# Kernel tuning notes

Measured on AMD Instinct MI355X. Metric: run time of the kernel, lower is better.

## Reference

```python
import jax, jax.numpy as jnp
import numpy as np

N_WORDS, L, VOCAB, D = 8192, 24, 128, 512
H, DK = 8, 64  # n_head, d_v (=d_k)
N_NAMES, WORDS_PER_NAME = 2048, 4
N_CONCEPTS, NAMES_PER_CONCEPT = 256, 8


def setup_inputs() -> dict:
    key = jax.random.key(0)
    ks = jax.random.split(key, 9)
    s = 1.0 / np.sqrt(D).astype(np.float32)
    inputs = jax.random.randint(ks[0], (N_WORDS, L), 0, VOCAB)  # 0 = pad char
    n_words = jnp.full((N_NAMES,), WORDS_PER_NAME, dtype=jnp.int32)
    n_names = jnp.full((N_CONCEPTS,), NAMES_PER_CONCEPT, dtype=jnp.int32)
    return {
        "inputs": inputs,
        "n_words": n_words,
        "n_names": n_names,
        "emb": jax.random.normal(ks[1], (VOCAB, D), jnp.float32) * s,
        "Wq": jax.random.normal(ks[2], (D, H * DK), jnp.float32) * s,
        "Wk": jax.random.normal(ks[3], (D, H * DK), jnp.float32) * s,
        "Wv": jax.random.normal(ks[4], (D, H * DK), jnp.float32) * s,
        "Wo": jax.random.normal(ks[5], (H * DK, D), jnp.float32) * s,
        "W1": jax.random.normal(ks[6], (D, 512), jnp.float32) * s,
        "W2": jax.random.normal(ks[7], (512, 256), jnp.float32) * s,
    }


def reference(inputs, n_words, n_names, emb, Wq, Wk, Wv, Wo, W1, W2):
    N, Lq = inputs.shape
    pad = inputs == 0  # [N, L] padding mask (char id 0)

    # --- MHAEncoder: embedding + masked multi-head self-attention ---
    x = emb[inputs]  # [N, L, D]
    def split_heads(t):  # [N, L, H*DK] -> [N, H, L, DK]
        return t.reshape(N, Lq, H, DK).transpose(0, 2, 1, 3)
    q = split_heads(x @ Wq)
    k = split_heads(x @ Wk)
    v = split_heads(x @ Wv)
    scale = jnp.asarray(1.0 / np.sqrt(DK), x.dtype)
    scores = jnp.einsum('nhqd,nhkd->nhqk', q, k) * scale  # [N, H, L, L]
    scores = jnp.where(pad[:, None, None, :], jnp.asarray(-1e9, x.dtype), scores)
    attn = jax.nn.softmax(scores, axis=-1)
    o = jnp.einsum('nhqk,nhkd->nhqd', attn, v)
    word_ft = o.transpose(0, 2, 1, 3).reshape(N, Lq, H * DK) @ Wo  # [N, L, D]

    # --- masked mean pooling over chars: matmul(mask, word_ft)/mask.sum(-1) ---
    m = (~pad).astype(word_ft.dtype)  # [N, L]
    name_emb = jnp.einsum('nl,nld->nd', m, word_ft) / m.sum(-1, keepdims=True)  # [N, D]

    # --- split(n_words) + per-group mean == segment mean over word groups ---
    G = n_words.shape[0]
    seg = jnp.repeat(jnp.arange(G), n_words, total_repeat_length=N)
    name_ft = jax.ops.segment_sum(name_emb, seg, num_segments=G)
    name_ft = name_ft / n_words[:, None].astype(name_ft.dtype)  # [G, D]

    # --- small no-bias Tanh MLP ---
    h = jnp.tanh(name_ft @ W1)
    out = jnp.tanh(h @ W2)  # [G, 256]
    # final .split(n_names) is a view-only regrouping; return the packed array
    return out
```

## Files before the change

### kernel.cpp

```cpp
#include <hip/hip_runtime.h>
#include <math.h>

#define NWORDS 8192
#define LW     24
#define VOC    128
#define DIM    512
#define NH     8
#define DKH    64
#define GNAMES 2048
#define F2     256

#define S1_LEN 458752
#define H1OFF  1048576

#define GEMM_BODY(A_, B_, K_, N_, m0_, n0_, kbeg_, kchunk_)                         \
  __shared__ float As[2][16][68];                                                   \
  __shared__ float Bs[2][16][68];                                                   \
  const int t = threadIdx.x, tx = t & 15, ty = t >> 4;                              \
  float acc[4][4] = {};                                                             \
  float ra[4], rb[4];                                                               \
  _Pragma("unroll")                                                                 \
  for (int i = 0; i < 4; ++i) { int idx = t + 256 * i;                              \
    ra[i] = A_[(size_t)(m0_ + (idx >> 4)) * K_ + kbeg_ + (idx & 15)]; }             \
  _Pragma("unroll")                                                                 \
  for (int i = 0; i < 4; ++i) { int idx = t + 256 * i;                              \
    rb[i] = B_[(size_t)(kbeg_ + (idx >> 6)) * N_ + n0_ + (idx & 63)]; }             \
  _Pragma("unroll")                                                                 \
  for (int i = 0; i < 4; ++i) { int idx = t + 256 * i; As[0][idx & 15][idx >> 4] = ra[i]; } \
  _Pragma("unroll")                                                                 \
  for (int i = 0; i < 4; ++i) { int idx = t + 256 * i; Bs[0][idx >> 6][idx & 63] = rb[i]; } \
  __syncthreads();                                                                  \
  int buf = 0;                                                                      \
  for (int k0 = kbeg_; k0 < kbeg_ + kchunk_; k0 += 16) {                            \
    const bool more = (k0 + 16 < kbeg_ + kchunk_);                                  \
    if (more) {                                                                     \
      _Pragma("unroll")                                                             \
      for (int i = 0; i < 4; ++i) { int idx = t + 256 * i;                          \
        ra[i] = A_[(size_t)(m0_ + (idx >> 4)) * K_ + (k0 + 16) + (idx & 15)]; }     \
      _Pragma("unroll")                                                             \
      for (int i = 0; i < 4; ++i) { int idx = t + 256 * i;                          \
        rb[i] = B_[(size_t)(k0 + 16 + (idx >> 6)) * N_ + n0_ + (idx & 63)]; }       \
    }                                                                               \
    _Pragma("unroll")                                                               \
    for (int k = 0; k < 16; ++k) {                                                  \
      float a[4], b[4];                                                             \
      _Pragma("unroll")                                                             \
      for (int i = 0; i < 4; ++i) a[i] = As[buf][k][ty * 4 + i];                    \
      _Pragma("unroll")                                                             \
      for (int j = 0; j < 4; ++j) b[j] = Bs[buf][k][tx * 4 + j];                    \
      _Pragma("unroll")                                                             \
      for (int i = 0; i < 4; ++i)                                                   \
        _Pragma("unroll")                                                           \
        for (int j = 0; j < 4; ++j) acc[i][j] += a[i] * b[j];                       \
    }                                                                               \
    if (more) {                                                                     \
      _Pragma("unroll")                                                             \
      for (int i = 0; i < 4; ++i) { int idx = t + 256 * i; As[buf ^ 1][idx & 15][idx >> 4] = ra[i]; } \
      _Pragma("unroll")                                                             \
      for (int i = 0; i < 4; ++i) { int idx = t + 256 * i; Bs[buf ^ 1][idx >> 6][idx & 63] = rb[i]; } \
      __syncthreads();                                                              \
      buf ^= 1;                                                                     \
    }                                                                               \
  }

template<int NSPLIT>
__global__ __launch_bounds__(256) void k_stage1(const float* __restrict__ emb,
                                                const float* __restrict__ Wq,
                                                const float* __restrict__ Wk,
                                                const float* __restrict__ Wv,
                                                const float* __restrict__ Wo,
                                                const float* __restrict__ W1,
                                                float* __restrict__ P) {
  const int tid = blockIdx.x, s = blockIdx.y;
  const float *A, *B;
  int coff, m0, n0;
  if (tid < 48) {
    const int g = tid >> 4, mt = tid & 15;
    A = emb;
    B = (g == 0) ? Wq : ((g == 1) ? Wk : Wv);
    coff = g * 65536;
    m0 = (mt >> 3) * 64; n0 = (mt & 7) * 64;
  } else {
    const int id = tid - 48;
    A = Wo; B = W1; coff = 3 * 65536;
    m0 = (id >> 3) * 64; n0 = (id & 7) * 64;
  }
  const int kchunk = 512 / NSPLIT, kbeg = s * kchunk;
  GEMM_BODY(A, B, 512, 512, m0, n0, kbeg, kchunk)
  float* Cp = P + (size_t)s * S1_LEN + coff;
  #pragma unroll
  for (int i = 0; i < 4; ++i) {
    float4 v = make_float4(acc[i][0], acc[i][1], acc[i][2], acc[i][3]);
    *(float4*)&Cp[(size_t)(m0 + ty * 4 + i) * 512 + n0 + tx * 4] = v;
  }
}

template<int ACT>
__global__ __launch_bounds__(256) void k_gemm64(const float* __restrict__ A,
                                                const float* __restrict__ B,
                                                float* __restrict__ C,
                                                int M, int N, int K, int kchunk) {
  const int m0 = blockIdx.y * 64, n0 = blockIdx.x * 64;
  const int kbeg = blockIdx.z * kchunk;
  GEMM_BODY(A, B, K, N, m0, n0, kbeg, kchunk)
  float* Cp = C + (size_t)blockIdx.z * M * N;
  #pragma unroll
  for (int i = 0; i < 4; ++i) {
    float4 v = make_float4(acc[i][0], acc[i][1], acc[i][2], acc[i][3]);
    if (ACT) { v.x = tanhf(v.x); v.y = tanhf(v.y); v.z = tanhf(v.z); v.w = tanhf(v.w); }
    *(float4*)&Cp[(size_t)(m0 + ty * 4 + i) * N + n0 + tx * 4] = v;
  }
}

__global__ __launch_bounds__(256) void k_npool(const float* __restrict__ Wn,
                                               const float* __restrict__ EV,
                                               float* __restrict__ NP) {
  const int m0 = blockIdx.x * 64, h = blockIdx.y;
  const float* A2 = Wn + (size_t)m0 * 1024 + h * 128;
  const float* B2 = EV + h * 64;
  GEMM_BODY(A2, B2, 1024, 512, 0, 0, 0, 128)
  #pragma unroll
  for (int i = 0; i < 4; ++i) {
    float4 v = make_float4(acc[i][0], acc[i][1], acc[i][2], acc[i][3]);
    *(float4*)&NP[(size_t)(m0 + ty * 4 + i) * 512 + h * 64 + tx * 4] = v;
  }
}

__global__ __launch_bounds__(256) void k_gemm_tail(const float* __restrict__ P,
                                                   const float* __restrict__ B,
                                                   float* __restrict__ C,
                                                   int kchunk) {
  const int N = 256, K = 512;
  __shared__ float As[2][16][68];
  __shared__ float Bs[2][16][68];
  const int t = threadIdx.x, tx = t & 15, ty = t >> 4;
  const int m0 = blockIdx.y * 64, n0 = blockIdx.x * 64;
  const int kbeg = blockIdx.z * kchunk;
  float acc[4][4] = {};
  float ra[4], rb[4];
  #pragma unroll
  for (int i = 0; i < 4; ++i) {
    int idx = t + 256 * i;
    size_t off = (size_t)(m0 + (idx >> 4)) * K + kbeg + (idx & 15);
    ra[i] = tanhf(P[off] + P[off + H1OFF] + P[off + 2 * H1OFF] + P[off + 3 * H1OFF]);
  }
  #pragma unroll
  for (int i = 0; i < 4; ++i) {
    int idx = t + 256 * i;
    rb[i] = B[(size_t)(kbeg + (idx >> 6)) * N + n0 + (idx & 63)];
  }
  #pragma unroll
  for (int i = 0; i < 4; ++i) { int idx = t + 256 * i; As[0][idx & 15][idx >> 4] = ra[i]; }
  #pragma unroll
  for (int i = 0; i < 4; ++i) { int idx = t + 256 * i; Bs[0][idx >> 6][idx & 63] = rb[i]; }
  __syncthreads();
  int buf = 0;
  for (int k0 = kbeg; k0 < kbeg + kchunk; k0 += 16) {
    const bool more = (k0 + 16 < kbeg + kchunk);
    if (more) {
      #pragma unroll
      for (int i = 0; i < 4; ++i) {
        int idx = t + 256 * i;
        size_t off = (size_t)(m0 + (idx >> 4)) * K + (k0 + 16) + (idx & 15);
        ra[i] = tanhf(P[off] + P[off + H1OFF] + P[off + 2 * H1OFF] + P[off + 3 * H1OFF]);
      }
      #pragma unroll
      for (int i = 0; i < 4; ++i) {
        int idx = t + 256 * i;
        rb[i] = B[(size_t)(k0 + 16 + (idx >> 6)) * N + n0 + (idx & 63)];
      }
    }
    #pragma unroll
    for (int k = 0; k < 16; ++k) {
      float a[4], b[4];
      #pragma unroll
      for (int i = 0; i < 4; ++i) a[i] = As[buf][k][ty * 4 + i];
      #pragma unroll
      for (int j = 0; j < 4; ++j) b[j] = Bs[buf][k][tx * 4 + j];
      #pragma unroll
      for (int i = 0; i < 4; ++i)
        #pragma unroll
        for (int j = 0; j < 4; ++j) acc[i][j] += a[i] * b[j];
    }
    if (more) {
      #pragma unroll
      for (int i = 0; i < 4; ++i) { int idx = t + 256 * i; As[buf ^ 1][idx & 15][idx >> 4] = ra[i]; }
      #pragma unroll
      for (int i = 0; i < 4; ++i) { int idx = t + 256 * i; Bs[buf ^ 1][idx >> 6][idx & 63] = rb[i]; }
      __syncthreads();
      buf ^= 1;
    }
  }
  float* Cp = C + (size_t)blockIdx.z * (GNAMES * F2);
  #pragma unroll
  for (int i = 0; i < 4; ++i) {
    float4 v = make_float4(acc[i][0], acc[i][1], acc[i][2], acc[i][3]);
    *(float4*)&Cp[(size_t)(m0 + ty * 4 + i) * N + n0 + tx * 4] = v;
  }
}

template<int ACT, int S>
__global__ __launch_bounds__(256) void k_reduce(const float* __restrict__ P,
                                                float* __restrict__ O,
                                                int len4, int stride4) {
  const int i = blockIdx.x * 256 + threadIdx.x;
  if (i >= len4) return;
  const float4* P4 = (const float4*)P;
  float4 a = P4[i];
  #pragma unroll
  for (int s = 1; s < S; ++s) {
    float4 b = P4[(size_t)s * stride4 + i];
    a.x += b.x; a.y += b.y; a.z += b.z; a.w += b.w;
  }
  if (ACT) { a.x = tanhf(a.x); a.y = tanhf(a.y); a.z = tanhf(a.z); a.w = tanhf(a.w); }
  ((float4*)O)[i] = a;
}

__global__ __launch_bounds__(128) void k_qk_tab(const float* __restrict__ EQ,
                                                const float* __restrict__ EK,
                                                float* __restrict__ etab) {
  const int c1 = blockIdx.x, h = blockIdx.y, c2 = threadIdx.x;
  __shared__ float qrow[DKH];
  if (threadIdx.x < DKH) qrow[threadIdx.x] = EQ[c1 * DIM + h * DKH + threadIdx.x];
  __syncthreads();
  const float* krow = EK + c2 * DIM + h * DKH;
  float acc = 0.f;
  #pragma unroll
  for (int d = 0; d < DKH; ++d) acc += qrow[d] * krow[d];
  float e = (c1 != 0 && c2 != 0) ? __expf(acc * 0.125f) : 0.f;
  etab[((size_t)c1 * VOC + c2) * NH + h] = e;
}

__global__ __launch_bounds__(256) void k_bins(const int* __restrict__ inputs,
                                              const int* __restrict__ nwords,
                                              const float* __restrict__ etab,
                                              float* __restrict__ Wn) {
  const int g = blockIdx.x, t = threadIdx.x;
  const int wv = t >> 6, l = t & 63;
  const int h = l & 7, qg = l >> 3;
  __shared__ float bins[VOC * NH];
  __shared__ int wred[4];
  __shared__ int sh_nwg;

  for (int i = t; i < VOC * NH; i += 256) bins[i] = 0.f;
  int partial = 0;
  for (int i = t; i < GNAMES; i += 256) {
    int v = nwords[i];
    partial += (i < g) ? v : 0;
    if (i == g) sh_nwg = v;
  }
  #pragma unroll
  for (int d = 1; d < 64; d <<= 1) partial += __shfl_xor(partial, d);
  if (l == 0) wred[wv] = partial;
  __syncthreads();
  const int nw = sh_nwg;
  const int o0 = wred[0] + wred[1] + wred[2] + wred[3];

  for (int wrel = wv; wrel < nw; wrel += 4) {
    const int wi = o0 + wrel;
    int c_l = (l < LW) ? inputs[(size_t)wi * LW + l] : 0;
    unsigned long long mk = __ballot(c_l != 0);
    int cnt = __popcll(mk);
    float invc = cnt ? 1.f / (float)cnt : 0.f;

    int cq0 = __shfl(c_l, qg);
    int cq1 = __shfl(c_l, qg + 8);
    int cq2 = __shfl(c_l, qg + 16);
    const float* b0 = etab + (cq0 << 10) + h;
    const float* b1 = etab + (cq1 << 10) + h;
    const float* b2 = etab + (cq2 << 10) + h;

    float r0[LW], r1[LW], r2[LW];
    float d0 = 0.f, d1 = 0.f, d2 = 0.f;
    #pragma unroll
    for (int kp = 0; kp < LW; ++kp) {
      int o = __shfl(c_l, kp) << 3;
      r0[kp] = b0[o]; r1[kp] = b1[o]; r2[kp] = b2[o];
      d0 += r0[kp]; d1 += r1[kp]; d2 += r2[kp];
    }
    float i0 = cq0 ? invc / d0 : 0.f;
    float i1 = cq1 ? invc / d1 : 0.f;
    float i2 = cq2 ? invc / d2 : 0.f;

    #pragma unroll
    for (int kp = 0; kp < LW; ++kp) {
      int ck = __shfl(c_l, kp);
      if (ck) {
        float v = r0[kp] * i0 + r1[kp] * i1 + r2[kp] * i2;
        v += __shfl_xor(v, 8);
        v += __shfl_xor(v, 16);
        v += __shfl_xor(v, 32);
        if (qg == 0) atomicAdd(&bins[(ck << 3) + h], v);
      }
    }
  }
  __syncthreads();

  const float invn = nw ? 1.f / (float)nw : 0.f;
  for (int i = t; i < NH * VOC; i += 256) {
    int hh = i >> 7, cc = i & 127;
    Wn[(size_t)g * 1024 + i] = bins[(cc << 3) + hh] * invn;
  }
}

extern "C" void kernel_launch(void* const* d_in, const int* in_sizes, int n_in,
                              void* d_out, int out_size, void* d_ws, size_t ws_size,
                              hipStream_t stream) {
  const int*   inputs  = (const int*)d_in[0];
  const int*   n_words = (const int*)d_in[1];
  const float* emb     = (const float*)d_in[3];
  const float* Wq      = (const float*)d_in[4];
  const float* Wk      = (const float*)d_in[5];
  const float* Wv      = (const float*)d_in[6];
  const float* Wo      = (const float*)d_in[7];
  const float* W1      = (const float*)d_in[8];
  const float* W2      = (const float*)d_in[9];
  float* out = (float*)d_out;

  float* ws   = (float*)d_ws;
  float* ES   = ws;
  float* BIG  = ws + 458752;
  float* TAB  = ws + 4653056;
  float* NP   = ws + 4784128;
  float* Wn   = ws + 5832704;
  float* OUTP = ws + 7929856;

  k_stage1<4><<<dim3(112, 4), 256, 0, stream>>>(emb, Wq, Wk, Wv, Wo, W1, BIG);
  k_reduce<0, 4><<<S1_LEN / 4 / 256, 256, 0, stream>>>(BIG, ES, S1_LEN / 4, S1_LEN / 4);
  k_qk_tab<<<dim3(VOC, NH), 128, 0, stream>>>(ES, ES + 65536, TAB);
  k_bins<<<GNAMES, 256, 0, stream>>>(inputs, n_words, TAB, Wn);
  k_npool<<<dim3(GNAMES / 64, NH), 256, 0, stream>>>(Wn, ES + 131072, NP);
  k_gemm64<0><<<dim3(8, 32, 4), 256, 0, stream>>>(NP, ES + 196608, BIG, 2048, 512, 512, 128);
  k_gemm_tail<<<dim3(4, 32, 4), 256, 0, stream>>>(BIG, W2, OUTP, 128);
  k_reduce<1, 4><<<(GNAMES * F2) / 4 / 256, 256, 0, stream>>>(OUTP, out, (GNAMES * F2) / 4, (GNAMES * F2) / 4);
}
```

Measured before the change: 107.0 us.

## Vectorize GEMM tile loads, deepen K tile to 32, raise stage-1 split-K

The shared fp32 GEMM body now moves global and LDS data with float4 accesses and steps K in tiles of 32 instead of 16, which halves the number of barriers per K chunk. The tanh-fused tail GEMM gets the same treatment through helper macros. Stage 1 moves from split-K 4 to 8 so more blocks are in flight, at the cost of a larger partial buffer to reduce. LDS per block doubles, which may lower occupancy, and the transposed scalar stores of A into LDS can hit bank conflicts.

```diff
diff --git a/kernel.cpp b/kernel.cpp
--- a/kernel.cpp
+++ b/kernel.cpp
@@ -13,51 +13,56 @@
 #define S1_LEN 458752
 #define H1OFF  1048576
 
-#define GEMM_BODY(A_, B_, K_, N_, m0_, n0_, kbeg_, kchunk_)                         \
-  __shared__ float As[2][16][68];                                                   \
-  __shared__ float Bs[2][16][68];                                                   \
+#define GEMM_BODY32(A_, B_, K_, N_, m0_, n0_, kbeg_, kchunk_)                       \
+  __shared__ float As[2][32][68];                                                   \
+  __shared__ float Bs[2][32][68];                                                   \
   const int t = threadIdx.x, tx = t & 15, ty = t >> 4;                              \
   float acc[4][4] = {};                                                             \
-  float ra[4], rb[4];                                                               \
-  _Pragma("unroll")                                                                 \
-  for (int i = 0; i < 4; ++i) { int idx = t + 256 * i;                              \
-    ra[i] = A_[(size_t)(m0_ + (idx >> 4)) * K_ + kbeg_ + (idx & 15)]; }             \
-  _Pragma("unroll")                                                                 \
-  for (int i = 0; i < 4; ++i) { int idx = t + 256 * i;                              \
-    rb[i] = B_[(size_t)(kbeg_ + (idx >> 6)) * N_ + n0_ + (idx & 63)]; }             \
-  _Pragma("unroll")                                                                 \
-  for (int i = 0; i < 4; ++i) { int idx = t + 256 * i; As[0][idx & 15][idx >> 4] = ra[i]; } \
-  _Pragma("unroll")                                                                 \
-  for (int i = 0; i < 4; ++i) { int idx = t + 256 * i; Bs[0][idx >> 6][idx & 63] = rb[i]; } \
+  float4 ra[2], rb[2];                                                              \
+  _Pragma("unroll")                                                                 \
+  for (int i = 0; i < 2; ++i) { int idx = t + 256 * i;                              \
+    ra[i] = *(const float4*)&A_[(size_t)(m0_ + (idx >> 3)) * K_ + kbeg_ + (idx & 7) * 4]; } \
+  _Pragma("unroll")                                                                 \
+  for (int i = 0; i < 2; ++i) { int idx = t + 256 * i;                              \
+    rb[i] = *(const float4*)&B_[(size_t)(kbeg_ + (idx >> 4)) * N_ + n0_ + (idx & 15) * 4]; } \
+  _Pragma("unroll")                                                                 \
+  for (int i = 0; i < 2; ++i) { int idx = t + 256 * i; int m = idx >> 3, k4 = (idx & 7) * 4; \
+    As[0][k4 + 0][m] = ra[i].x; As[0][k4 + 1][m] = ra[i].y;                         \
+    As[0][k4 + 2][m] = ra[i].z; As[0][k4 + 3][m] = ra[i].w; }                       \
+  _Pragma("unroll")                                                                 \
+  for (int i = 0; i < 2; ++i) { int idx = t + 256 * i;                              \
+    *(float4*)&Bs[0][idx >> 4][(idx & 15) * 4] = rb[i]; }                           \
   __syncthreads();                                                                  \
   int buf = 0;                                                                      \
-  for (int k0 = kbeg_; k0 < kbeg_ + kchunk_; k0 += 16) {                            \
-    const bool more = (k0 + 16 < kbeg_ + kchunk_);                                  \
+  for (int k0 = kbeg_; k0 < kbeg_ + kchunk_; k0 += 32) {                            \
+    const bool more = (k0 + 32 < kbeg_ + kchunk_);                                  \
     if (more) {                                                                     \
       _Pragma("unroll")                                                             \
-      for (int i = 0; i < 4; ++i) { int idx = t + 256 * i;                          \
-        ra[i] = A_[(size_t)(m0_ + (idx >> 4)) * K_ + (k0 + 16) + (idx & 15)]; }     \
+      for (int i = 0; i < 2; ++i) { int idx = t + 256 * i;                          \
+        ra[i] = *(const float4*)&A_[(size_t)(m0_ + (idx >> 3)) * K_ + (k0 + 32) + (idx & 7) * 4]; } \
       _Pragma("unroll")                                                             \
-      for (int i = 0; i < 4; ++i) { int idx = t + 256 * i;                          \
-        rb[i] = B_[(size_t)(k0 + 16 + (idx >> 6)) * N_ + n0_ + (idx & 63)]; }       \
+      for (int i = 0; i < 2; ++i) { int idx = t + 256 * i;                          \
+        rb[i] = *(const float4*)&B_[(size_t)(k0 + 32 + (idx >> 4)) * N_ + n0_ + (idx & 15) * 4]; } \
     }                                                                               \
     _Pragma("unroll")                                                               \
-    for (int k = 0; k < 16; ++k) {                                                  \
-      float a[4], b[4];                                                             \
-      _Pragma("unroll")                                                             \
-      for (int i = 0; i < 4; ++i) a[i] = As[buf][k][ty * 4 + i];                    \
-      _Pragma("unroll")                                                             \
-      for (int j = 0; j < 4; ++j) b[j] = Bs[buf][k][tx * 4 + j];                    \
-      _Pragma("unroll")                                                             \
-      for (int i = 0; i < 4; ++i)                                                   \
-        _Pragma("unroll")                                                           \
-        for (int j = 0; j < 4; ++j) acc[i][j] += a[i] * b[j];                       \
+    for (int k = 0; k < 32; ++k) {                                                  \
+      float4 av = *(const float4*)&As[buf][k][ty * 4];                              \
+      float4 bv = *(const float4*)&Bs[buf][k][tx * 4];                              \
+      float a0 = av.x, a1 = av.y, a2 = av.z, a3 = av.w;                             \
+      float b0 = bv.x, b1 = bv.y, b2 = bv.z, b3 = bv.w;                             \
+      acc[0][0] += a0 * b0; acc[0][1] += a0 * b1; acc[0][2] += a0 * b2; acc[0][3] += a0 * b3; \
+      acc[1][0] += a1 * b0; acc[1][1] += a1 * b1; acc[1][2] += a1 * b2; acc[1][3] += a1 * b3; \
+      acc[2][0] += a2 * b0; acc[2][1] += a2 * b1; acc[2][2] += a2 * b2; acc[2][3] += a2 * b3; \
+      acc[3][0] += a3 * b0; acc[3][1] += a3 * b1; acc[3][2] += a3 * b2; acc[3][3] += a3 * b3; \
     }                                                                               \
     if (more) {                                                                     \
       _Pragma("unroll")                                                             \
-      for (int i = 0; i < 4; ++i) { int idx = t + 256 * i; As[buf ^ 1][idx & 15][idx >> 4] = ra[i]; } \
+      for (int i = 0; i < 2; ++i) { int idx = t + 256 * i; int m = idx >> 3, k4 = (idx & 7) * 4; \
+        As[buf ^ 1][k4 + 0][m] = ra[i].x; As[buf ^ 1][k4 + 1][m] = ra[i].y;         \
+        As[buf ^ 1][k4 + 2][m] = ra[i].z; As[buf ^ 1][k4 + 3][m] = ra[i].w; }       \
       _Pragma("unroll")                                                             \
-      for (int i = 0; i < 4; ++i) { int idx = t + 256 * i; Bs[buf ^ 1][idx >> 6][idx & 63] = rb[i]; } \
+      for (int i = 0; i < 2; ++i) { int idx = t + 256 * i;                          \
+        *(float4*)&Bs[buf ^ 1][idx >> 4][(idx & 15) * 4] = rb[i]; }                 \
       __syncthreads();                                                              \
       buf ^= 1;                                                                     \
     }                                                                               \
@@ -86,7 +91,7 @@
     m0 = (id >> 3) * 64; n0 = (id & 7) * 64;
   }
   const int kchunk = 512 / NSPLIT, kbeg = s * kchunk;
-  GEMM_BODY(A, B, 512, 512, m0, n0, kbeg, kchunk)
+  GEMM_BODY32(A, B, 512, 512, m0, n0, kbeg, kchunk)
   float* Cp = P + (size_t)s * S1_LEN + coff;
   #pragma unroll
   for (int i = 0; i < 4; ++i) {
@@ -102,7 +107,7 @@
                                                 int M, int N, int K, int kchunk) {
   const int m0 = blockIdx.y * 64, n0 = blockIdx.x * 64;
   const int kbeg = blockIdx.z * kchunk;
-  GEMM_BODY(A, B, K, N, m0, n0, kbeg, kchunk)
+  GEMM_BODY32(A, B, K, N, m0, n0, kbeg, kchunk)
   float* Cp = C + (size_t)blockIdx.z * M * N;
   #pragma unroll
   for (int i = 0; i < 4; ++i) {
@@ -118,7 +123,7 @@
   const int m0 = blockIdx.x * 64, h = blockIdx.y;
   const float* A2 = Wn + (size_t)m0 * 1024 + h * 128;
   const float* B2 = EV + h * 64;
-  GEMM_BODY(A2, B2, 1024, 512, 0, 0, 0, 128)
+  GEMM_BODY32(A2, B2, 1024, 512, 0, 0, 0, 128)
   #pragma unroll
   for (int i = 0; i < 4; ++i) {
     float4 v = make_float4(acc[i][0], acc[i][1], acc[i][2], acc[i][3]);
@@ -131,65 +136,59 @@
                                                    float* __restrict__ C,
                                                    int kchunk) {
   const int N = 256, K = 512;
-  __shared__ float As[2][16][68];
-  __shared__ float Bs[2][16][68];
+  __shared__ float As[2][32][68];
+  __shared__ float Bs[2][32][68];
   const int t = threadIdx.x, tx = t & 15, ty = t >> 4;
   const int m0 = blockIdx.y * 64, n0 = blockIdx.x * 64;
   const int kbeg = blockIdx.z * kchunk;
   float acc[4][4] = {};
-  float ra[4], rb[4];
-  #pragma unroll
-  for (int i = 0; i < 4; ++i) {
-    int idx = t + 256 * i;
-    size_t off = (size_t)(m0 + (idx >> 4)) * K + kbeg + (idx & 15);
-    ra[i] = tanhf(P[off] + P[off + H1OFF] + P[off + 2 * H1OFF] + P[off + 3 * H1OFF]);
-  }
-  #pragma unroll
-  for (int i = 0; i < 4; ++i) {
-    int idx = t + 256 * i;
-    rb[i] = B[(size_t)(kbeg + (idx >> 6)) * N + n0 + (idx & 63)];
-  }
-  #pragma unroll
-  for (int i = 0; i < 4; ++i) { int idx = t + 256 * i; As[0][idx & 15][idx >> 4] = ra[i]; }
-  #pragma unroll
-  for (int i = 0; i < 4; ++i) { int idx = t + 256 * i; Bs[0][idx >> 6][idx & 63] = rb[i]; }
+  float4 ra[2], rb[2];
+#define TAIL_LOAD_A(kb)                                                             \
+  _Pragma("unroll")                                                                 \
+  for (int i = 0; i < 2; ++i) {                                                     \
+    int idx = t + 256 * i;                                                          \
+    size_t off = (size_t)(m0 + (idx >> 3)) * K + (kb) + (idx & 7) * 4;              \
+    float4 p0 = *(const float4*)&P[off];                                            \
+    float4 p1 = *(const float4*)&P[off + H1OFF];                                    \
+    float4 p2 = *(const float4*)&P[off + 2 * H1OFF];                                \
+    float4 p3 = *(const float4*)&P[off + 3 * H1OFF];                                \
+    ra[i].x = tanhf(p0.x + p1.x + p2.x + p3.x);                                     \
+    ra[i].y = tanhf(p0.y + p1.y + p2.y + p3.y);                                     \
+    ra[i].z = tanhf(p0.z + p1.z + p2.z + p3.z);                                     \
+    ra[i].w = tanhf(p0.w + p1.w + p2.w + p3.w);                                     \
+  }
+#define TAIL_LOAD_B(kb)                                                             \
+  _Pragma("unroll")                                                                 \
+  for (int i = 0; i < 2; ++i) { int idx = t + 256 * i;                              \
+    rb[i] = *(const float4*)&B[(size_t)((kb) + (idx >> 4)) * N + n0 + (idx & 15) * 4]; }
+#define TAIL_STORE(bb)                                                              \
+  _Pragma("unroll")                                                                 \
+  for (int i = 0; i < 2; ++i) { int idx = t + 256 * i; int m = idx >> 3, k4 = (idx & 7) * 4; \
+    As[bb][k4 + 0][m] = ra[i].x; As[bb][k4 + 1][m] = ra[i].y;                       \
+    As[bb][k4 + 2][m] = ra[i].z; As[bb][k4 + 3][m] = ra[i].w; }                     \
+  _Pragma("unroll")                                                                 \
+  for (int i = 0; i < 2; ++i) { int idx = t + 256 * i;                              \
+    *(float4*)&Bs[bb][idx >> 4][(idx & 15) * 4] = rb[i]; }
+  TAIL_LOAD_A(kbeg)
+  TAIL_LOAD_B(kbeg)
+  TAIL_STORE(0)
   __syncthreads();
   int buf = 0;
-  for (int k0 = kbeg; k0 < kbeg + kchunk; k0 += 16) {
-    const bool more = (k0 + 16 < kbeg + kchunk);
-    if (more) {
-      #pragma unroll
-      for (int i = 0; i < 4; ++i) {
-        int idx = t + 256 * i;
-        size_t off = (size_t)(m0 + (idx >> 4)) * K + (k0 + 16) + (idx & 15);
-        ra[i] = tanhf(P[off] + P[off + H1OFF] + P[off + 2 * H1OFF] + P[off + 3 * H1OFF]);
-      }
-      #pragma unroll
-      for (int i = 0; i < 4; ++i) {
-        int idx = t + 256 * i;
-        rb[i] = B[(size_t)(k0 + 16 + (idx >> 6)) * N + n0 + (idx & 63)];
-      }
+  for (int k0 = kbeg; k0 < kbeg + kchunk; k0 += 32) {
+    const bool more = (k0 + 32 < kbeg + kchunk);
+    if (more) { TAIL_LOAD_A(k0 + 32) TAIL_LOAD_B(k0 + 32) }
+    #pragma unroll
+    for (int k = 0; k < 32; ++k) {
+      float4 av = *(const float4*)&As[buf][k][ty * 4];
+      float4 bv = *(const float4*)&Bs[buf][k][tx * 4];
+      float a0 = av.x, a1 = av.y, a2 = av.z, a3 = av.w;
+      float b0 = bv.x, b1 = bv.y, b2 = bv.z, b3 = bv.w;
+      acc[0][0] += a0 * b0; acc[0][1] += a0 * b1; acc[0][2] += a0 * b2; acc[0][3] += a0 * b3;
+      acc[1][0] += a1 * b0; acc[1][1] += a1 * b1; acc[1][2] += a1 * b2; acc[1][3] += a1 * b3;
+      acc[2][0] += a2 * b0; acc[2][1] += a2 * b1; acc[2][2] += a2 * b2; acc[2][3] += a2 * b3;
+      acc[3][0] += a3 * b0; acc[3][1] += a3 * b1; acc[3][2] += a3 * b2; acc[3][3] += a3 * b3;
     }
-    #pragma unroll
-    for (int k = 0; k < 16; ++k) {
-      float a[4], b[4];
-      #pragma unroll
-      for (int i = 0; i < 4; ++i) a[i] = As[buf][k][ty * 4 + i];
-      #pragma unroll
-      for (int j = 0; j < 4; ++j) b[j] = Bs[buf][k][tx * 4 + j];
-      #pragma unroll
-      for (int i = 0; i < 4; ++i)
-        #pragma unroll
-        for (int j = 0; j < 4; ++j) acc[i][j] += a[i] * b[j];
-    }
-    if (more) {
-      #pragma unroll
-      for (int i = 0; i < 4; ++i) { int idx = t + 256 * i; As[buf ^ 1][idx & 15][idx >> 4] = ra[i]; }
-      #pragma unroll
-      for (int i = 0; i < 4; ++i) { int idx = t + 256 * i; Bs[buf ^ 1][idx >> 6][idx & 63] = rb[i]; }
-      __syncthreads();
-      buf ^= 1;
-    }
+    if (more) { TAIL_STORE(buf ^ 1) __syncthreads(); buf ^= 1; }
   }
   float* Cp = C + (size_t)blockIdx.z * (GNAMES * F2);
   #pragma unroll
@@ -325,8 +324,8 @@
   float* Wn   = ws + 5832704;
   float* OUTP = ws + 7929856;
 
-  k_stage1<4><<<dim3(112, 4), 256, 0, stream>>>(emb, Wq, Wk, Wv, Wo, W1, BIG);
-  k_reduce<0, 4><<<S1_LEN / 4 / 256, 256, 0, stream>>>(BIG, ES, S1_LEN / 4, S1_LEN / 4);
+  k_stage1<8><<<dim3(112, 8), 256, 0, stream>>>(emb, Wq, Wk, Wv, Wo, W1, BIG);
+  k_reduce<0, 8><<<S1_LEN / 4 / 256, 256, 0, stream>>>(BIG, ES, S1_LEN / 4, S1_LEN / 4);
   k_qk_tab<<<dim3(VOC, NH), 128, 0, stream>>>(ES, ES + 65536, TAB);
   k_bins<<<GNAMES, 256, 0, stream>>>(inputs, n_words, TAB, Wn);
   k_npool<<<dim3(GNAMES / 64, NH), 256, 0, stream>>>(Wn, ES + 131072, NP);
```

Result: slower. 120.7 us (+12.8%).
